# Kernel optimization log

Hardware: AMD Instinct MI355X
Metric: run time of the kernel (lower is better)

The kernel has to match this reference:

```python
import jax, jax.numpy as jnp
import numpy as np

B, T, H, E = 128, 512, 512, 512
V_IN, V_OUT = 50000, 30000


def setup_inputs() -> dict:
    key = jax.random.key(0)
    ks = jax.random.split(key, 24)
    f = jax.random.normal
    stdv = 1.0 / np.sqrt(H)
    return {
        "inputs": jax.random.randint(ks[0], (B,), 0, V_IN),
        "last_hidden": f(ks[1], (1, B, H), dtype=jnp.float32),
        "code_outputs": f(ks[2], (T, B, H), dtype=jnp.float32),
        "ast_outputs": f(ks[3], (T, B, H), dtype=jnp.float32),
        "code_coverage": jax.random.uniform(ks[4], (B, T), dtype=jnp.float32),
        "ast_coverage": jax.random.uniform(ks[5], (B, T), dtype=jnp.float32),
        "embedding": f(ks[6], (V_IN, E)) * 0.01,
        "code_W_attn": f(ks[7], (H, 3 * H)) * 0.02,
        "code_b_attn": f(ks[8], (H,)) * 0.01,
        "code_v": f(ks[9], (H,)) * stdv,
        "code_W_cov": f(ks[10], (H,)) * 0.02,
        "ast_W_attn": f(ks[11], (H, 3 * H)) * 0.02,
        "ast_b_attn": f(ks[12], (H,)) * 0.01,
        "ast_v": f(ks[13], (H,)) * stdv,
        "ast_W_cov": f(ks[14], (H,)) * 0.02,
        "gru_W_ih": f(ks[15], (3 * H, E + H)) * 0.02,
        "gru_W_hh": f(ks[16], (3 * H, H)) * 0.02,
        "gru_b_ih": f(ks[17], (3 * H,)) * 0.01,
        "gru_b_hh": f(ks[18], (3 * H,)) * 0.01,
        "W_out": f(ks[19], (V_OUT, 2 * H)) * 0.01,
        "b_out": f(ks[20], (V_OUT,)) * 0.01,
    }


def _attention(hidden, enc, cov, W, b, v, Wc):
    # hidden [B,H], enc [T,B,H], cov [B,T]; Wc is the [H] weight of Linear(1,H,bias=False)
    encb = jnp.swapaxes(enc, 0, 1)  # [B,T,H]
    h = jnp.broadcast_to(hidden[:, None, :], encb.shape)  # [B,T,H]
    cov_feat = cov[:, :, None] * Wc  # [B,T,H]
    feat = jnp.concatenate([h, encb, cov_feat], axis=2)  # [B,T,3H]
    energy = jax.nn.relu(feat @ W.T + b)  # [B,T,H]
    scores = energy @ v  # [B,T]
    w = jax.nn.softmax(scores, axis=1)  # softmax over T
    return w, cov + w


def reference(inputs, last_hidden, code_outputs, ast_outputs, code_coverage,
              ast_coverage, embedding, code_W_attn, code_b_attn, code_v,
              code_W_cov, ast_W_attn, ast_b_attn, ast_v, ast_W_cov,
              gru_W_ih, gru_W_hh, gru_b_ih, gru_b_hh, W_out, b_out):
    h0 = last_hidden[0]  # [B,H]
    emb = embedding[inputs]  # [B,E]

    cw, ccov = _attention(h0, code_outputs, code_coverage,
                          code_W_attn, code_b_attn, code_v, code_W_cov)
    aw, acov = _attention(h0, ast_outputs, ast_coverage,
                          ast_W_attn, ast_b_attn, ast_v, ast_W_cov)

    code_ctx = jnp.einsum('bt,tbh->bh', cw, code_outputs)
    ast_ctx = jnp.einsum('bt,tbh->bh', aw, ast_outputs)
    ctx = 0.5 * (code_ctx + ast_ctx)  # [B,H]

    # one-step GRU (PyTorch gate layout: r, z, n)
    x = jnp.concatenate([emb, ctx], axis=1)  # [B,E+H]
    gi = x @ gru_W_ih.T + gru_b_ih
    gh = h0 @ gru_W_hh.T + gru_b_hh
    i_r, i_z, i_n = jnp.split(gi, 3, axis=1)
    h_r, h_z, h_n = jnp.split(gh, 3, axis=1)
    r = jax.nn.sigmoid(i_r + h_r)
    z = jax.nn.sigmoid(i_z + h_z)
    n = jnp.tanh(i_n + r * h_n)
    h1 = (1.0 - z) * n + z * h0  # [B,H]

    logits = jnp.concatenate([h1, ctx], axis=1) @ W_out.T + b_out  # [B,V_OUT]
    out = jax.nn.log_softmax(logits, axis=1)
    return (out, h1[None], cw[:, None, :], aw[:, None, :], ccov, acov)
```

## Files before the change

kernel.cpp:

```cpp
#include <hip/hip_runtime.h>
#include <math.h>

#define B_ 128
#define T_ 512
#define H_ 512
#define E_ 512
#define VOUT 30000
#define M_ (T_*B_)

typedef __attribute__((ext_vector_type(8))) short short8;
typedef __attribute__((ext_vector_type(4))) float f32x4;

__device__ __forceinline__ ushort f2b(float f) {
    union { float f; unsigned int i; } c; c.f = f;
    unsigned int x = c.i;
    unsigned int r = (x + 0x7FFFu + ((x >> 16) & 1u)) >> 16;
    return (ushort)r;
}
__device__ __forceinline__ short8 cvt8(const float* p) {
    float4 a = *(const float4*)p;
    float4 b = *(const float4*)(p + 4);
    unsigned int r0, r1, r2, r3;
    asm("v_cvt_pk_bf16_f32 %0, %1, %2" : "=v"(r0) : "v"(a.x), "v"(a.y));
    asm("v_cvt_pk_bf16_f32 %0, %1, %2" : "=v"(r1) : "v"(a.z), "v"(a.w));
    asm("v_cvt_pk_bf16_f32 %0, %1, %2" : "=v"(r2) : "v"(b.x), "v"(b.y));
    asm("v_cvt_pk_bf16_f32 %0, %1, %2" : "=v"(r3) : "v"(b.z), "v"(b.w));
    union { unsigned int u[4]; short8 s; } u;
    u.u[0] = r0; u.u[1] = r1; u.u[2] = r2; u.u[3] = r3;
    return u.s;
}


__global__ void emb_gather(const int* idx, const float* emb, float* x) {
    int b = blockIdx.x; int t = threadIdx.x;
    int row = idx[b];
    x[b*1024 + t]       = emb[(size_t)row*E_ + t];
    x[b*1024 + t + 256] = emb[(size_t)row*E_ + t + 256];
}

__global__ void prep_a1(const float* h0, const float* Wc, const float* bc,
                        const float* Wa, const float* ba, float* A1) {
    int b = blockIdx.x; int which = blockIdx.y;
    const float* W    = which ? Wa : Wc;
    const float* bias = which ? ba : bc;
    __shared__ float hs[H_];
    for (int k = threadIdx.x; k < H_; k += 256) hs[k] = h0[b*H_ + k];
    __syncthreads();
    for (int h = threadIdx.x; h < H_; h += 256) {
        const float* Wr = W + (size_t)h * 1536;
        float s = 0.f;
        for (int k = 0; k < H_; k += 4) {
            float4 w = *(const float4*)(Wr + k);
            s += hs[k]*w.x + hs[k+1]*w.y + hs[k+2]*w.z + hs[k+3]*w.w;
        }
        A1[((size_t)which*B_ + b)*H_ + h] = s + bias[h];
    }
}

__global__ void prep_u(const float* wcov_c, const float* W_c,
                       const float* wcov_a, const float* W_a, float* u) {
    int which = blockIdx.x; int h = threadIdx.x;
    const float* W  = which ? W_a : W_c;
    const float* wc = which ? wcov_a : wcov_c;
    const float* Wr = W + (size_t)h*1536 + 1024;
    float s = 0.f;
    for (int k = 0; k < H_; ++k) s += wc[k] * Wr[k];
    u[which*H_ + h] = s;
}


#define BK 64
#define LDSS 72

__global__ __launch_bounds__(256)
void attn_gemm(const float* code_enc, const float* ast_enc,
               const float* code_W, const float* ast_W,
               const float* code_v, const float* ast_v,
               const float* code_cov, const float* ast_cov,
               const float* A1, const float* u, float* scores) {
    int which = blockIdx.y;
    const float* enc = which ? ast_enc : code_enc;
    const float* W   = which ? ast_W   : code_W;
    const float* vv  = which ? ast_v   : code_v;
    const float* cov = which ? ast_cov : code_cov;
    const float* A1w = A1 + (size_t)which * B_ * H_;
    const float* uw  = u + which * H_;
    float* sc = scores + (size_t)which * M_;

    int bid = blockIdx.x;
    int tile = ((bid & 7) << 8) + (bid >> 3);
    int mt = tile >> 2, nt = tile & 3;
    int m0 = mt * 128, n0 = nt * 128;

    __shared__ __align__(16) ushort As[128 * LDSS];
    __shared__ __align__(16) ushort Bs[128 * LDSS];

    int tid = threadIdx.x;
    int lane = tid & 63, wave = tid >> 6;
    int wm = wave >> 1, wn = wave & 1;
    int col = lane & 15, quad = lane >> 4;

    f32x4 acc[4][4];
    #pragma unroll
    for (int i = 0; i < 4; ++i)
        #pragma unroll
        for (int j = 0; j < 4; ++j) acc[i][j] = (f32x4)(0.f);

    for (int k0 = 0; k0 < H_; k0 += BK) {
        __syncthreads();
        #pragma unroll
        for (int it = 0; it < 4; ++it) {
            int c = it * 256 + tid;
            int row = c >> 3, c8 = (c & 7) * 8;
            *(short8*)(&As[row * LDSS + c8]) =
                cvt8(enc + (size_t)(m0 + row) * H_ + k0 + c8);
            *(short8*)(&Bs[row * LDSS + c8]) =
                cvt8(W + (size_t)(n0 + row) * 1536 + 512 + k0 + c8);
        }
        __syncthreads();
        #pragma unroll
        for (int kk = 0; kk < BK; kk += 32) {
            short8 af[4], bfr[4];
            #pragma unroll
            for (int i = 0; i < 4; ++i)
                af[i] = *(const short8*)(&As[(wm*64 + i*16 + col) * LDSS + kk + quad*8]);
            #pragma unroll
            for (int j = 0; j < 4; ++j)
                bfr[j] = *(const short8*)(&Bs[(wn*64 + j*16 + col) * LDSS + kk + quad*8]);
            #pragma unroll
            for (int i = 0; i < 4; ++i)
                #pragma unroll
                for (int j = 0; j < 4; ++j)
                    acc[i][j] = __builtin_amdgcn_mfma_f32_16x16x32_bf16(af[i], bfr[j], acc[i][j], 0, 0, 0);
        }
    }

    float u4[4], v4[4]; int h4[4];
    #pragma unroll
    for (int j = 0; j < 4; ++j) {
        int h = n0 + wn*64 + j*16 + col;
        h4[j] = h; u4[j] = uw[h]; v4[j] = vv[h];
    }
    #pragma unroll
    for (int i = 0; i < 4; ++i) {
        #pragma unroll
        for (int r = 0; r < 4; ++r) {
            int mg = m0 + wm*64 + i*16 + quad*4 + r;
            int b = mg & (B_-1), t = mg >> 7;
            float cv = cov[b*T_ + t];
            float s = 0.f;
            #pragma unroll
            for (int j = 0; j < 4; ++j) {
                float val = acc[i][j][r] + A1w[b*H_ + h4[j]] + cv * u4[j];
                val = val > 0.f ? val : 0.f;
                s += val * v4[j];
            }
            #pragma unroll
            for (int off = 1; off < 16; off <<= 1) s += __shfl_xor(s, off, 64);
            if (col == 0) atomicAdd(&sc[mg], s);
        }
    }
}

__global__ void attn_softmax(const float* scores, const float* code_cov, const float* ast_cov,
                             float* wsm, float* out) {
    int b = blockIdx.x, which = blockIdx.y;
    const float* sc = scores + (size_t)which * M_;
    const float* cov = which ? ast_cov : code_cov;
    float* wrow = wsm + ((size_t)which * B_ + b) * T_;
    float* w_out   = out + 3840000 + 65536 + (size_t)which * 65536 + b * T_;
    float* cov_out = out + 3840000 + 65536 + 131072 + (size_t)which * 65536 + b * T_;
    int tid = threadIdx.x;
    __shared__ float red[8];
    float v0 = sc[tid * B_ + b];
    float v1 = sc[(tid + 256) * B_ + b];
    float m = fmaxf(v0, v1);
    #pragma unroll
    for (int off = 32; off; off >>= 1) m = fmaxf(m, __shfl_xor(m, off, 64));
    if ((tid & 63) == 0) red[tid >> 6] = m;
    __syncthreads();
    m = fmaxf(fmaxf(red[0], red[1]), fmaxf(red[2], red[3]));
    float e0 = expf(v0 - m), e1 = expf(v1 - m);
    float s = e0 + e1;
    #pragma unroll
    for (int off = 32; off; off >>= 1) s += __shfl_xor(s, off, 64);
    if ((tid & 63) == 0) red[4 + (tid >> 6)] = s;
    __syncthreads();
    float inv = 1.f / (red[4] + red[5] + red[6] + red[7]);
    float w0 = e0 * inv, w1 = e1 * inv;
    wrow[tid] = w0; wrow[tid + 256] = w1;
    w_out[tid] = w0; w_out[tid + 256] = w1;
    cov_out[tid]       = cov[b*T_ + tid]       + w0;
    cov_out[tid + 256] = cov[b*T_ + tid + 256] + w1;
}

__global__ void ctx_kernel(const float* code_enc, const float* ast_enc,
                           const float* wsm, float* x) {
    int b = blockIdx.x, tc = blockIdx.y;
    int tid = threadIdx.x;
    __shared__ float wc[128], wa[128];
    if (tid < 128) {
        wc[tid] = wsm[(size_t)b * T_ + tc*128 + tid];
        wa[tid] = wsm[(size_t)(B_ + b) * T_ + tc*128 + tid];
    }
    __syncthreads();
    float a0 = 0.f, a1 = 0.f;
    for (int i = 0; i < 128; ++i) {
        int t = tc * 128 + i;
        float2 c2 = *(const float2*)(code_enc + (size_t)t * (B_*H_) + b*H_ + tid*2);
        float2 a2 = *(const float2*)(ast_enc  + (size_t)t * (B_*H_) + b*H_ + tid*2);
        a0 += wc[i]*c2.x + wa[i]*a2.x;
        a1 += wc[i]*c2.y + wa[i]*a2.y;
    }
    atomicAdd(&x[b*1024 + 512 + tid*2],     0.5f*a0);
    atomicAdd(&x[b*1024 + 512 + tid*2 + 1], 0.5f*a1);
}

__global__ void gru_gemm(const float* x, const float* h0, const float* Wih, const float* Whh,
                         const float* bih, const float* bhh, float* g) {
    int blk = blockIdx.x;
    int b = blk / 6, c = blk % 6;
    int tid = threadIdx.x;
    __shared__ float xs[1024];
    __shared__ float hs[512];
    for (int k = tid; k < 1024; k += 256) xs[k] = x[b*1024 + k];
    for (int k = tid; k < 512; k += 256)  hs[k] = h0[b*512 + k];
    __syncthreads();
    int n = c*256 + tid;
    const float* wi = Wih + (size_t)n * 1024;
    const float* wh = Whh + (size_t)n * 512;
    float si = 0.f, sh = 0.f;
    for (int k = 0; k < 1024; k += 4) {
        float4 w = *(const float4*)(wi + k);
        si += xs[k]*w.x + xs[k+1]*w.y + xs[k+2]*w.z + xs[k+3]*w.w;
    }
    for (int k = 0; k < 512; k += 4) {
        float4 w = *(const float4*)(wh + k);
        sh += hs[k]*w.x + hs[k+1]*w.y + hs[k+2]*w.z + hs[k+3]*w.w;
    }
    si += bih[n]; sh += bhh[n];
    int gate = n >> 9, h = n & 511;
    if (gate == 0)      g[b*512 + h] = si + sh;
    else if (gate == 1) g[65536 + b*512 + h] = si + sh;
    else { g[131072 + b*512 + h] = si;
           g[196608 + b*512 + h] = sh; }
}

__global__ void gru_finish(const float* g, const float* x, const float* h0,
                           float* out, float* y) {
    int i = blockIdx.x * 256 + threadIdx.x;
    int b = i >> 9, h = i & 511;
    float r = 1.f / (1.f + expf(-g[i]));
    float z = 1.f / (1.f + expf(-g[65536 + i]));
    float nn = tanhf(g[131072 + i] + r * g[196608 + i]);
    float h1 = (1.f - z) * nn + z * h0[i];
    out[3840000 + i] = h1;
    y[b*1024 + h]       = h1;
    y[b*1024 + 512 + h] = x[b*1024 + 512 + h];
}

__global__ __launch_bounds__(256)
void logits_gemm(const float* y, const float* Wout, const float* bout, float* out0) {
    int n0 = blockIdx.x * 128;
    __shared__ __align__(16) ushort As[128 * LDSS];
    __shared__ __align__(16) ushort Bs[128 * LDSS];
    int tid = threadIdx.x, lane = tid & 63, wave = tid >> 6;
    int wm = wave >> 1, wn = wave & 1;
    int col = lane & 15, quad = lane >> 4;
    f32x4 acc[4][4];
    #pragma unroll
    for (int i = 0; i < 4; ++i)
        #pragma unroll
        for (int j = 0; j < 4; ++j) acc[i][j] = (f32x4)(0.f);

    for (int k0 = 0; k0 < 1024; k0 += BK) {
        __syncthreads();
        #pragma unroll
        for (int it = 0; it < 4; ++it) {
            int c = it * 256 + tid;
            int row = c >> 3, c8 = (c & 7) * 8;
            *(short8*)(&As[row * LDSS + c8]) =
                cvt8(y + (size_t)row * 1024 + k0 + c8);
            int brow = n0 + row; if (brow > VOUT-1) brow = VOUT-1;
            *(short8*)(&Bs[row * LDSS + c8]) =
                cvt8(Wout + (size_t)brow * 1024 + k0 + c8);
        }
        __syncthreads();
        #pragma unroll
        for (int kk = 0; kk < BK; kk += 32) {
            short8 af[4], bfr[4];
            #pragma unroll
            for (int i = 0; i < 4; ++i)
                af[i] = *(const short8*)(&As[(wm*64 + i*16 + col) * LDSS + kk + quad*8]);
            #pragma unroll
            for (int j = 0; j < 4; ++j)
                bfr[j] = *(const short8*)(&Bs[(wn*64 + j*16 + col) * LDSS + kk + quad*8]);
            #pragma unroll
            for (int i = 0; i < 4; ++i)
                #pragma unroll
                for (int j = 0; j < 4; ++j)
                    acc[i][j] = __builtin_amdgcn_mfma_f32_16x16x32_bf16(af[i], bfr[j], acc[i][j], 0, 0, 0);
        }
    }
    #pragma unroll
    for (int i = 0; i < 4; ++i)
        #pragma unroll
        for (int j = 0; j < 4; ++j) {
            int h = n0 + wn*64 + j*16 + col;
            if (h < VOUT) {
                float bo = bout[h];
                #pragma unroll
                for (int r = 0; r < 4; ++r) {
                    int m = wm*64 + i*16 + quad*4 + r;
                    out0[(size_t)m * VOUT + h] = acc[i][j][r] + bo;
                }
            }
        }
}

__global__ void logsoftmax(float* out0) {
    int b = blockIdx.x; int tid = threadIdx.x;
    float* row = out0 + (size_t)b * VOUT;
    __shared__ float red[8];
    float m = -1e30f;
    for (int i = tid; i < VOUT; i += 256) m = fmaxf(m, row[i]);
    #pragma unroll
    for (int off = 32; off; off >>= 1) m = fmaxf(m, __shfl_xor(m, off, 64));
    if ((tid & 63) == 0) red[tid >> 6] = m;
    __syncthreads();
    m = fmaxf(fmaxf(red[0], red[1]), fmaxf(red[2], red[3]));
    float s = 0.f;
    for (int i = tid; i < VOUT; i += 256) s += expf(row[i] - m);
    #pragma unroll
    for (int off = 32; off; off >>= 1) s += __shfl_xor(s, off, 64);
    if ((tid & 63) == 0) red[4 + (tid >> 6)] = s;
    __syncthreads();
    float lse = m + logf(red[4] + red[5] + red[6] + red[7]);
    for (int i = tid; i < VOUT; i += 256) row[i] = row[i] - lse;
}

extern "C" void kernel_launch(void* const* d_in, const int* in_sizes, int n_in,
                              void* d_out, int out_size, void* d_ws, size_t ws_size,
                              hipStream_t stream) {
    const int*   inputs   = (const int*)d_in[0];
    const float* h0       = (const float*)d_in[1];
    const float* code_enc = (const float*)d_in[2];
    const float* ast_enc  = (const float*)d_in[3];
    const float* code_cov = (const float*)d_in[4];
    const float* ast_cov  = (const float*)d_in[5];
    const float* emb      = (const float*)d_in[6];
    const float* code_W   = (const float*)d_in[7];
    const float* code_b   = (const float*)d_in[8];
    const float* code_v   = (const float*)d_in[9];
    const float* code_Wc  = (const float*)d_in[10];
    const float* ast_W    = (const float*)d_in[11];
    const float* ast_b    = (const float*)d_in[12];
    const float* ast_v    = (const float*)d_in[13];
    const float* ast_Wc   = (const float*)d_in[14];
    const float* gru_Wih  = (const float*)d_in[15];
    const float* gru_Whh  = (const float*)d_in[16];
    const float* gru_bih  = (const float*)d_in[17];
    const float* gru_bhh  = (const float*)d_in[18];
    const float* W_out    = (const float*)d_in[19];
    const float* b_out    = (const float*)d_in[20];
    float* out = (float*)d_out;

    char* ws = (char*)d_ws;
    float* scores = (float*)(ws + 0);
    float* x      = (float*)(ws + 524288);
    float* A1     = (float*)(ws + 1048576);
    float* wsm    = (float*)(ws + 1572864);
    float* u      = (float*)(ws + 2097152);
    float* g      = (float*)(ws + 2101248);
    float* y      = (float*)(ws + 3149824);

    hipMemsetAsync(ws, 0, 1048576, stream);

    emb_gather<<<dim3(B_), dim3(256), 0, stream>>>(inputs, emb, x);
    prep_a1<<<dim3(B_, 2), dim3(256), 0, stream>>>(h0, code_W, code_b, ast_W, ast_b, A1);
    prep_u<<<dim3(2), dim3(512), 0, stream>>>(code_Wc, code_W, ast_Wc, ast_W, u);

    attn_gemm<<<dim3(2048, 2), dim3(256), 0, stream>>>(
        code_enc, ast_enc, code_W, ast_W, code_v, ast_v, code_cov, ast_cov, A1, u, scores);

    attn_softmax<<<dim3(B_, 2), dim3(256), 0, stream>>>(scores, code_cov, ast_cov, wsm, out);

    ctx_kernel<<<dim3(B_, 4), dim3(256), 0, stream>>>(code_enc, ast_enc, wsm, x);

    gru_gemm<<<dim3(768), dim3(256), 0, stream>>>(x, h0, gru_Wih, gru_Whh, gru_bih, gru_bhh, g);
    gru_finish<<<dim3(256), dim3(256), 0, stream>>>(g, x, h0, out, y);

    logits_gemm<<<dim3(235), dim3(256), 0, stream>>>(y, W_out, b_out, out);
    logsoftmax<<<dim3(B_), dim3(256), 0, stream>>>(out);
}
```

Before: 955.4 us.

## Restructure attention GEMM to full-N tiles and batch-block the small GEMV kernels

The attention GEMM now uses 1024-thread blocks that each cover all 512 hidden columns for a 128-row tile. Global loads are register-prefetched one k-step ahead, and per-row score partials are reduced in LDS. This removes the atomics and the scores memset, and each encoder tile is converted to bf16 once instead of four times. prep_a1 and gru_gemm now process several batch rows per block so each weight load is reused, and ctx_kernel switches to float4 loads over finer time chunks. The larger block and LDS footprint in attn_gemm may reduce occupancy.

Measured after the change: 857.7 us. 10.2% less time.

```diff
diff --git a/kernel.cpp b/kernel.cpp
--- a/kernel.cpp
+++ b/kernel.cpp
@@ -11,15 +11,7 @@
 typedef __attribute__((ext_vector_type(8))) short short8;
 typedef __attribute__((ext_vector_type(4))) float f32x4;
 
-__device__ __forceinline__ ushort f2b(float f) {
-    union { float f; unsigned int i; } c; c.f = f;
-    unsigned int x = c.i;
-    unsigned int r = (x + 0x7FFFu + ((x >> 16) & 1u)) >> 16;
-    return (ushort)r;
-}
-__device__ __forceinline__ short8 cvt8(const float* p) {
-    float4 a = *(const float4*)p;
-    float4 b = *(const float4*)(p + 4);
+__device__ __forceinline__ short8 cvt8v(float4 a, float4 b) {
     unsigned int r0, r1, r2, r3;
     asm("v_cvt_pk_bf16_f32 %0, %1, %2" : "=v"(r0) : "v"(a.x), "v"(a.y));
     asm("v_cvt_pk_bf16_f32 %0, %1, %2" : "=v"(r1) : "v"(a.z), "v"(a.w));
@@ -29,6 +21,9 @@
     u.u[0] = r0; u.u[1] = r1; u.u[2] = r2; u.u[3] = r3;
     return u.s;
 }
+__device__ __forceinline__ short8 cvt8(const float* p) {
+    return cvt8v(*(const float4*)p, *(const float4*)(p + 4));
+}
 
 
 __global__ void emb_gather(const int* idx, const float* emb, float* x) {
@@ -38,23 +33,41 @@
     x[b*1024 + t + 256] = emb[(size_t)row*E_ + t + 256];
 }
 
-__global__ void prep_a1(const float* h0, const float* Wc, const float* bc,
+__global__ void prep_a1(const float* h0, const float* Wc, const float* bc_,
                         const float* Wa, const float* ba, float* A1) {
-    int b = blockIdx.x; int which = blockIdx.y;
+    int hc = blockIdx.x;
+    int bcb = blockIdx.y;
+    int which = blockIdx.z;
     const float* W    = which ? Wa : Wc;
-    const float* bias = which ? ba : bc;
-    __shared__ float hs[H_];
-    for (int k = threadIdx.x; k < H_; k += 256) hs[k] = h0[b*H_ + k];
-    __syncthreads();
-    for (int h = threadIdx.x; h < H_; h += 256) {
-        const float* Wr = W + (size_t)h * 1536;
-        float s = 0.f;
-        for (int k = 0; k < H_; k += 4) {
-            float4 w = *(const float4*)(Wr + k);
-            s += hs[k]*w.x + hs[k+1]*w.y + hs[k+2]*w.z + hs[k+3]*w.w;
-        }
-        A1[((size_t)which*B_ + b)*H_ + h] = s + bias[h];
-    }
+    const float* bias = which ? ba : bc_;
+    int b0 = bcb * 16;
+    int tid = threadIdx.x;
+    __shared__ float hs[16][512];
+    for (int idx = tid; idx < 2048; idx += 256) {
+        int row = idx >> 7, c = (idx & 127) * 4;
+        *(float4*)&hs[row][c] = *(const float4*)(h0 + (size_t)(b0+row)*512 + c);
+    }
+    __syncthreads();
+    int h = hc*64 + (tid & 63);
+    int r = (tid >> 6) * 4;
+    const float* Wr = W + (size_t)h * 1536;
+    float a0=0.f, a1=0.f, a2=0.f, a3=0.f;
+    for (int k = 0; k < 512; k += 4) {
+        float4 w  = *(const float4*)(Wr + k);
+        float4 x0 = *(const float4*)&hs[r][k];
+        float4 x1 = *(const float4*)&hs[r+1][k];
+        float4 x2 = *(const float4*)&hs[r+2][k];
+        float4 x3 = *(const float4*)&hs[r+3][k];
+        a0 += w.x*x0.x + w.y*x0.y + w.z*x0.z + w.w*x0.w;
+        a1 += w.x*x1.x + w.y*x1.y + w.z*x1.z + w.w*x1.w;
+        a2 += w.x*x2.x + w.y*x2.y + w.z*x2.z + w.w*x2.w;
+        a3 += w.x*x3.x + w.y*x3.y + w.z*x3.z + w.w*x3.w;
+    }
+    float bb = bias[h];
+    A1[((size_t)which*B_ + (b0+r  ))*H_ + h] = a0 + bb;
+    A1[((size_t)which*B_ + (b0+r+1))*H_ + h] = a1 + bb;
+    A1[((size_t)which*B_ + (b0+r+2))*H_ + h] = a2 + bb;
+    A1[((size_t)which*B_ + (b0+r+3))*H_ + h] = a3 + bb;
 }
 
 __global__ void prep_u(const float* wcov_c, const float* W_c,
@@ -72,7 +85,7 @@
 #define BK 64
 #define LDSS 72
 
-__global__ __launch_bounds__(256)
+__global__ __launch_bounds__(1024)
 void attn_gemm(const float* code_enc, const float* ast_enc,
                const float* code_W, const float* ast_W,
                const float* code_v, const float* ast_v,
@@ -88,45 +101,65 @@
     float* sc = scores + (size_t)which * M_;
 
     int bid = blockIdx.x;
-    int tile = ((bid & 7) << 8) + (bid >> 3);
-    int mt = tile >> 2, nt = tile & 3;
-    int m0 = mt * 128, n0 = nt * 128;
+    int mt  = ((bid & 7) << 6) + (bid >> 3);
+    int m0  = mt * 128;
 
     __shared__ __align__(16) ushort As[128 * LDSS];
-    __shared__ __align__(16) ushort Bs[128 * LDSS];
+    __shared__ __align__(16) ushort Bs[512 * LDSS];
+    __shared__ float red[128][8];
 
     int tid = threadIdx.x;
     int lane = tid & 63, wave = tid >> 6;
-    int wm = wave >> 1, wn = wave & 1;
+    int wm2 = wave >> 3, wn8 = wave & 7;
     int col = lane & 15, quad = lane >> 4;
 
+    int arow = tid >> 3, ac8 = (tid & 7) * 8;
+    const float* asrc = enc + (size_t)(m0 + arow) * H_ + ac8;
+    const float* bsrc = W + (size_t)arow * 1536 + 512 + ac8;
+
     f32x4 acc[4][4];
     #pragma unroll
     for (int i = 0; i < 4; ++i)
         #pragma unroll
         for (int j = 0; j < 4; ++j) acc[i][j] = (f32x4)(0.f);
 
-    for (int k0 = 0; k0 < H_; k0 += BK) {
+    float4 ra0, ra1, rb[8];
+    ra0 = *(const float4*)(asrc);
+    ra1 = *(const float4*)(asrc + 4);
+    #pragma unroll
+    for (int it = 0; it < 4; ++it) {
+        const float* p = bsrc + (size_t)it * 196608;
+        rb[2*it]   = *(const float4*)(p);
+        rb[2*it+1] = *(const float4*)(p + 4);
+    }
+
+    for (int kt = 0; kt < 8; ++kt) {
         __syncthreads();
-        #pragma unroll
-        for (int it = 0; it < 4; ++it) {
-            int c = it * 256 + tid;
-            int row = c >> 3, c8 = (c & 7) * 8;
-            *(short8*)(&As[row * LDSS + c8]) =
-                cvt8(enc + (size_t)(m0 + row) * H_ + k0 + c8);
-            *(short8*)(&Bs[row * LDSS + c8]) =
-                cvt8(W + (size_t)(n0 + row) * 1536 + 512 + k0 + c8);
-        }
+        *(short8*)(&As[arow * LDSS + ac8]) = cvt8v(ra0, ra1);
+        #pragma unroll
+        for (int it = 0; it < 4; ++it)
+            *(short8*)(&Bs[(it*128 + arow) * LDSS + ac8]) = cvt8v(rb[2*it], rb[2*it+1]);
         __syncthreads();
+        if (kt < 7) {
+            int k0 = (kt + 1) * BK;
+            ra0 = *(const float4*)(asrc + k0);
+            ra1 = *(const float4*)(asrc + k0 + 4);
+            #pragma unroll
+            for (int it = 0; it < 4; ++it) {
+                const float* p = bsrc + (size_t)it * 196608 + k0;
+                rb[2*it]   = *(const float4*)(p);
+                rb[2*it+1] = *(const float4*)(p + 4);
+            }
+        }
         #pragma unroll
         for (int kk = 0; kk < BK; kk += 32) {
             short8 af[4], bfr[4];
             #pragma unroll
             for (int i = 0; i < 4; ++i)
-                af[i] = *(const short8*)(&As[(wm*64 + i*16 + col) * LDSS + kk + quad*8]);
+                af[i] = *(const short8*)(&As[(wm2*64 + i*16 + col) * LDSS + kk + quad*8]);
             #pragma unroll
             for (int j = 0; j < 4; ++j)
-                bfr[j] = *(const short8*)(&Bs[(wn*64 + j*16 + col) * LDSS + kk + quad*8]);
+                bfr[j] = *(const short8*)(&Bs[(wn8*64 + j*16 + col) * LDSS + kk + quad*8]);
             #pragma unroll
             for (int i = 0; i < 4; ++i)
                 #pragma unroll
@@ -138,16 +171,15 @@
     float u4[4], v4[4]; int h4[4];
     #pragma unroll
     for (int j = 0; j < 4; ++j) {
-        int h = n0 + wn*64 + j*16 + col;
+        int h = wn8*64 + j*16 + col;
         h4[j] = h; u4[j] = uw[h]; v4[j] = vv[h];
     }
     #pragma unroll
     for (int i = 0; i < 4; ++i) {
         #pragma unroll
         for (int r = 0; r < 4; ++r) {
-            int mg = m0 + wm*64 + i*16 + quad*4 + r;
-            int b = mg & (B_-1), t = mg >> 7;
-            float cv = cov[b*T_ + t];
+            int b = wm2*64 + i*16 + quad*4 + r;
+            float cv = cov[b*T_ + mt];
             float s = 0.f;
             #pragma unroll
             for (int j = 0; j < 4; ++j) {
@@ -157,23 +189,30 @@
             }
             #pragma unroll
             for (int off = 1; off < 16; off <<= 1) s += __shfl_xor(s, off, 64);
-            if (col == 0) atomicAdd(&sc[mg], s);
-        }
+            if (col == 0) red[b][wn8] = s;
+        }
+    }
+    __syncthreads();
+    if (tid < 128) {
+        float s = 0.f;
+        #pragma unroll
+        for (int w = 0; w < 8; ++w) s += red[tid][w];
+        sc[(size_t)tid * T_ + mt] = s;
     }
 }
 
 __global__ void attn_softmax(const float* scores, const float* code_cov, const float* ast_cov,
                              float* wsm, float* out) {
     int b = blockIdx.x, which = blockIdx.y;
-    const float* sc = scores + (size_t)which * M_;
+    const float* sc = scores + (size_t)which * M_ + (size_t)b * T_;
     const float* cov = which ? ast_cov : code_cov;
     float* wrow = wsm + ((size_t)which * B_ + b) * T_;
     float* w_out   = out + 3840000 + 65536 + (size_t)which * 65536 + b * T_;
     float* cov_out = out + 3840000 + 65536 + 131072 + (size_t)which * 65536 + b * T_;
     int tid = threadIdx.x;
     __shared__ float red[8];
-    float v0 = sc[tid * B_ + b];
-    float v1 = sc[(tid + 256) * B_ + b];
+    float v0 = sc[tid];
+    float v1 = sc[tid + 256];
     float m = fmaxf(v0, v1);
     #pragma unroll
     for (int off = 32; off; off >>= 1) m = fmaxf(m, __shfl_xor(m, off, 64));
@@ -198,52 +237,81 @@
                            const float* wsm, float* x) {
     int b = blockIdx.x, tc = blockIdx.y;
     int tid = threadIdx.x;
-    __shared__ float wc[128], wa[128];
-    if (tid < 128) {
-        wc[tid] = wsm[(size_t)b * T_ + tc*128 + tid];
-        wa[tid] = wsm[(size_t)(B_ + b) * T_ + tc*128 + tid];
-    }
-    __syncthreads();
-    float a0 = 0.f, a1 = 0.f;
-    for (int i = 0; i < 128; ++i) {
-        int t = tc * 128 + i;
-        float2 c2 = *(const float2*)(code_enc + (size_t)t * (B_*H_) + b*H_ + tid*2);
-        float2 a2 = *(const float2*)(ast_enc  + (size_t)t * (B_*H_) + b*H_ + tid*2);
-        a0 += wc[i]*c2.x + wa[i]*a2.x;
-        a1 += wc[i]*c2.y + wa[i]*a2.y;
-    }
-    atomicAdd(&x[b*1024 + 512 + tid*2],     0.5f*a0);
-    atomicAdd(&x[b*1024 + 512 + tid*2 + 1], 0.5f*a1);
+    __shared__ float wc[64], wa[64];
+    if (tid < 64) {
+        wc[tid] = wsm[(size_t)b * T_ + tc*64 + tid];
+        wa[tid] = wsm[(size_t)(B_ + b) * T_ + tc*64 + tid];
+    }
+    __syncthreads();
+    float a0=0.f, a1=0.f, a2=0.f, a3=0.f;
+    for (int i = 0; i < 64; ++i) {
+        int t = tc * 64 + i;
+        float4 c4 = *(const float4*)(code_enc + (size_t)t * (B_*H_) + b*H_ + tid*4);
+        float4 a4 = *(const float4*)(ast_enc  + (size_t)t * (B_*H_) + b*H_ + tid*4);
+        a0 += wc[i]*c4.x + wa[i]*a4.x;
+        a1 += wc[i]*c4.y + wa[i]*a4.y;
+        a2 += wc[i]*c4.z + wa[i]*a4.z;
+        a3 += wc[i]*c4.w + wa[i]*a4.w;
+    }
+    atomicAdd(&x[b*1024 + 512 + tid*4],     0.5f*a0);
+    atomicAdd(&x[b*1024 + 512 + tid*4 + 1], 0.5f*a1);
+    atomicAdd(&x[b*1024 + 512 + tid*4 + 2], 0.5f*a2);
+    atomicAdd(&x[b*1024 + 512 + tid*4 + 3], 0.5f*a3);
 }
 
 __global__ void gru_gemm(const float* x, const float* h0, const float* Wih, const float* Whh,
                          const float* bih, const float* bhh, float* g) {
-    int blk = blockIdx.x;
-    int b = blk / 6, c = blk % 6;
+    int nc = blockIdx.x;
+    int bcb = blockIdx.y;
+    int b0 = bcb * 8;
     int tid = threadIdx.x;
-    __shared__ float xs[1024];
-    __shared__ float hs[512];
-    for (int k = tid; k < 1024; k += 256) xs[k] = x[b*1024 + k];
-    for (int k = tid; k < 512; k += 256)  hs[k] = h0[b*512 + k];
-    __syncthreads();
-    int n = c*256 + tid;
+    __shared__ float xs[8][1024];
+    __shared__ float hs[8][512];
+    for (int idx = tid; idx < 2048; idx += 256) {
+        int row = idx >> 8, c = (idx & 255) * 4;
+        *(float4*)&xs[row][c] = *(const float4*)(x + (size_t)(b0+row)*1024 + c);
+    }
+    for (int idx = tid; idx < 1024; idx += 256) {
+        int row = idx >> 7, c = (idx & 127) * 4;
+        *(float4*)&hs[row][c] = *(const float4*)(h0 + (size_t)(b0+row)*512 + c);
+    }
+    __syncthreads();
+    int n = nc * 64 + (tid & 63);
+    int r0 = (tid >> 6) * 2, r1 = r0 + 1;
     const float* wi = Wih + (size_t)n * 1024;
     const float* wh = Whh + (size_t)n * 512;
-    float si = 0.f, sh = 0.f;
+    float si0=0.f, si1=0.f, sh0=0.f, sh1=0.f;
     for (int k = 0; k < 1024; k += 4) {
-        float4 w = *(const float4*)(wi + k);
-        si += xs[k]*w.x + xs[k+1]*w.y + xs[k+2]*w.z + xs[k+3]*w.w;
+        float4 w  = *(const float4*)(wi + k);
+        float4 x0 = *(const float4*)&xs[r0][k];
+        float4 x1 = *(const float4*)&xs[r1][k];
+        si0 += w.x*x0.x + w.y*x0.y + w.z*x0.z + w.w*x0.w;
+        si1 += w.x*x1.x + w.y*x1.y + w.z*x1.z + w.w*x1.w;
     }
     for (int k = 0; k < 512; k += 4) {
-        float4 w = *(const float4*)(wh + k);
-        sh += hs[k]*w.x + hs[k+1]*w.y + hs[k+2]*w.z + hs[k+3]*w.w;
-    }
-    si += bih[n]; sh += bhh[n];
+        float4 w  = *(const float4*)(wh + k);
+        float4 x0 = *(const float4*)&hs[r0][k];
+        float4 x1 = *(const float4*)&hs[r1][k];
+        sh0 += w.x*x0.x + w.y*x0.y + w.z*x0.z + w.w*x0.w;
+        sh1 += w.x*x1.x + w.y*x1.y + w.z*x1.z + w.w*x1.w;
+    }
     int gate = n >> 9, h = n & 511;
-    if (gate == 0)      g[b*512 + h] = si + sh;
-    else if (gate == 1) g[65536 + b*512 + h] = si + sh;
-    else { g[131072 + b*512 + h] = si;
-           g[196608 + b*512 + h] = sh; }
+    float bi = bih[n], bh = bhh[n];
+    int b;
+    b = b0 + r0;
+    {
+        float A = si0 + bi, Bv = sh0 + bh;
+        if (gate == 0)      g[b*512 + h] = A + Bv;
+        else if (gate == 1) g[65536 + b*512 + h] = A + Bv;
+        else { g[131072 + b*512 + h] = A; g[196608 + b*512 + h] = Bv; }
+    }
+    b = b0 + r1;
+    {
+        float A = si1 + bi, Bv = sh1 + bh;
+        if (gate == 0)      g[b*512 + h] = A + Bv;
+        else if (gate == 1) g[65536 + b*512 + h] = A + Bv;
+        else { g[131072 + b*512 + h] = A; g[196608 + b*512 + h] = Bv; }
+    }
 }
 
 __global__ void gru_finish(const float* g, const float* x, const float* h0,
@@ -374,20 +442,20 @@
     float* g      = (float*)(ws + 2101248);
     float* y      = (float*)(ws + 3149824);
 
-    hipMemsetAsync(ws, 0, 1048576, stream);
+    hipMemsetAsync(ws + 524288, 0, 524288, stream);
 
     emb_gather<<<dim3(B_), dim3(256), 0, stream>>>(inputs, emb, x);
-    prep_a1<<<dim3(B_, 2), dim3(256), 0, stream>>>(h0, code_W, code_b, ast_W, ast_b, A1);
+    prep_a1<<<dim3(8, 8, 2), dim3(256), 0, stream>>>(h0, code_W, code_b, ast_W, ast_b, A1);
     prep_u<<<dim3(2), dim3(512), 0, stream>>>(code_Wc, code_W, ast_Wc, ast_W, u);
 
-    attn_gemm<<<dim3(2048, 2), dim3(256), 0, stream>>>(
+    attn_gemm<<<dim3(512, 2), dim3(1024), 0, stream>>>(
         code_enc, ast_enc, code_W, ast_W, code_v, ast_v, code_cov, ast_cov, A1, u, scores);
 
     attn_softmax<<<dim3(B_, 2), dim3(256), 0, stream>>>(scores, code_cov, ast_cov, wsm, out);
 
-    ctx_kernel<<<dim3(B_, 4), dim3(256), 0, stream>>>(code_enc, ast_enc, wsm, x);
-
-    gru_gemm<<<dim3(768), dim3(256), 0, stream>>>(x, h0, gru_Wih, gru_Whh, gru_bih, gru_bhh, g);
+    ctx_kernel<<<dim3(B_, 8), dim3(128), 0, stream>>>(code_enc, ast_enc, wsm, x);
+
+    gru_gemm<<<dim3(24, 16), dim3(256), 0, stream>>>(x, h0, gru_Wih, gru_Whh, gru_bih, gru_bhh, g);
     gru_finish<<<dim3(256), dim3(256), 0, stream>>>(g, x, h0, out, y);
 
     logits_gemm<<<dim3(235), dim3(256), 0, stream>>>(y, W_out, b_out, out);
```
